# Performance work log

Measured on AMD Instinct MI355X. Metric: run time of the kernel, lower is better.

Reference implementation:

```python
import jax, jax.numpy as jnp
import numpy as np

G, T, V, K = 24, 2048, 2048, 512  # group size, seq len, vocab, hidden


def setup_inputs() -> dict:
    key = jax.random.key(0)
    k1, k2, k3, k4 = jax.random.split(key, 4)
    # one-hot input sequence (T, V), batch squeezed away as in the torch code
    tokens = jax.random.randint(k1, (T,), 0, V)
    sequence = jax.nn.one_hot(tokens, V, dtype=jnp.float32)
    # group represented as V-permutations (one per group element); cyclic shifts
    # give a valid faithful permutation representation for the reference
    perms = (jnp.arange(V)[None, :] + jnp.arange(G)[:, None] * (V // G)) % V
    W_e = jax.random.normal(k2, (V, K), jnp.float32) * 0.02          # WordConv embedding table
    Wx = jax.random.normal(k3, (K, K), jnp.float32) / np.sqrt(K)     # input-to-hidden (shared across g)
    Wh = jax.random.normal(k4, (K, K), jnp.float32) / np.sqrt(K)     # hidden-to-hidden (shared across g)
    b = jnp.zeros((K,), jnp.float32)
    return {"sequence": sequence, "perms": perms, "W_e": W_e, "Wx": Wx, "Wh": Wh, "b": b}


def _forward_pass(xproj, Wh):
    # xproj: (T, G, K) pre-computed input projections; GRNN recurrence per group copy
    h0 = jnp.zeros(xproj.shape[1:], xproj.dtype)  # (G, K)

    def step(h, x):
        h = jnp.tanh(x + h @ Wh)
        return h, h

    hT, hs = jax.lax.scan(step, h0, xproj)
    return hs, hT  # (T, G, K), (G, K)


def reference(sequence, perms, W_e, Wx, Wh, b):
    # WordConv group embedding: emb[t, g] = W_e[perm_g(token_t)] via one-hot matmul
    emb = jnp.einsum('tv,gvk->tgk', sequence, W_e[perms])  # (T, G, K)
    xproj = jnp.einsum('tgk,kh->tgh', emb, Wx) + b         # hoist input GEMM out of the scan
    hid_f, ht_f = _forward_pass(xproj, Wh)
    # bidirectional: reverse = cat(seq[:-1].flip(0), seq[-1][None]) exactly as in torch
    rev = jnp.concatenate([xproj[:-1][::-1], xproj[-1:]], axis=0)
    hid_b, ht_b = _forward_pass(rev, Wh)
    hid_b = jnp.concatenate([hid_b[:-1][::-1], hid_b[-1:]], axis=0)
    hidden_all = jnp.concatenate([hid_f, hid_b], axis=-1)  # (T, G, 2K)
    ht = jnp.concatenate([ht_f, ht_b], axis=-1)            # (G, 2K)
    return hidden_all, ht
```

## Files before the change

### kernel.cpp

```cpp
#include <hip/hip_runtime.h>

#define T_LEN 2048
#define G_N   24
#define V_N   2048
#define K_N   512
#define NCL   48
#define NBLK  96

#define TOK_OFF    4096
#define ROWS_OFF   16384
#define HBUF_OFF   262144
#define P_OFF      786432

#define LOAD_RLX64(p)     __hip_atomic_load((p), __ATOMIC_RELAXED, __HIP_MEMORY_SCOPE_AGENT)
#define STORE_RLX64(p, v) __hip_atomic_store((p), (v), __ATOMIC_RELAXED, __HIP_MEMORY_SCOPE_AGENT)

#define BAR_LDS() do {                                         \
    asm volatile("s_waitcnt lgkmcnt(0)" ::: "memory");         \
    __builtin_amdgcn_s_barrier();                              \
    asm volatile("" ::: "memory");                             \
} while (0)

__global__ void tok_kernel(const float* __restrict__ seq, int* __restrict__ tokens) {
    int wid  = (blockIdx.x * blockDim.x + threadIdx.x) >> 6;
    int lane = threadIdx.x & 63;
    if (wid >= T_LEN) return;
    const float* row = seq + (size_t)wid * V_N;
    for (int i = lane; i < V_N; i += 64) {
        if (row[i] > 0.5f) tokens[wid] = i;
    }
}

__global__ void rows_kernel(const int* __restrict__ tokens, const int* __restrict__ perms,
                            int* __restrict__ rows) {
    int idx = blockIdx.x * blockDim.x + threadIdx.x;
    if (idx >= G_N * T_LEN) return;
    int g = idx / T_LEN, t = idx - g * T_LEN;
    rows[idx] = perms[g * V_N + tokens[t]];
}

__global__ __launch_bounds__(256) void pgemm_kernel(const float* __restrict__ We,
                                                    const float* __restrict__ Wx,
                                                    const float* __restrict__ b,
                                                    float* __restrict__ P) {
    __shared__ float As[16][72];
    __shared__ float Bs[16][68];
    int tid = threadIdx.x;
    int bx = blockIdx.x & 7;
    int by = blockIdx.x >> 3;
    int tx = tid & 15, ty = tid >> 4;
    int v0 = by * 64, j0 = bx * 64;
    float acc[4][4] = {};
    for (int k0 = 0; k0 < K_N; k0 += 16) {
        int ar = tid >> 2;
        int ac = (tid & 3) << 2;
        float4 av = *(const float4*)(We + (size_t)(v0 + ar) * K_N + k0 + ac);
        As[ac + 0][ar] = av.x; As[ac + 1][ar] = av.y;
        As[ac + 2][ar] = av.z; As[ac + 3][ar] = av.w;
        int br = tid >> 4;
        int bc = (tid & 15) << 2;
        float4 bv = *(const float4*)(Wx + (size_t)(k0 + br) * K_N + j0 + bc);
        *(float4*)&Bs[br][bc] = bv;
        __syncthreads();
#pragma unroll
        for (int kk = 0; kk < 16; kk++) {
            float a0 = As[kk][ty * 4 + 0], a1 = As[kk][ty * 4 + 1];
            float a2 = As[kk][ty * 4 + 2], a3 = As[kk][ty * 4 + 3];
            float4 bb = *(const float4*)&Bs[kk][tx * 4];
            acc[0][0] += a0 * bb.x; acc[0][1] += a0 * bb.y; acc[0][2] += a0 * bb.z; acc[0][3] += a0 * bb.w;
            acc[1][0] += a1 * bb.x; acc[1][1] += a1 * bb.y; acc[1][2] += a1 * bb.z; acc[1][3] += a1 * bb.w;
            acc[2][0] += a2 * bb.x; acc[2][1] += a2 * bb.y; acc[2][2] += a2 * bb.z; acc[2][3] += a2 * bb.w;
            acc[3][0] += a3 * bb.x; acc[3][1] += a3 * bb.y; acc[3][2] += a3 * bb.z; acc[3][3] += a3 * bb.w;
        }
        __syncthreads();
    }
    float4 bb = *(const float4*)(b + j0 + tx * 4);
#pragma unroll
    for (int i = 0; i < 4; i++) {
        float4 r;
        r.x = acc[i][0] + bb.x; r.y = acc[i][1] + bb.y;
        r.z = acc[i][2] + bb.z; r.w = acc[i][3] + bb.w;
        *(float4*)(P + (size_t)(v0 + ty * 4 + i) * K_N + j0 + tx * 4) = r;
    }
}

__global__ __attribute__((amdgpu_flat_work_group_size(512, 512), amdgpu_waves_per_eu(2, 2)))
void rnn_pair(const float* __restrict__ P, const float* __restrict__ Wh,
              const int* __restrict__ rows, unsigned long long* __restrict__ h_buf,
              float* __restrict__ out) {

    __shared__ __align__(16) float  lds_h[K_N];
    __shared__ __align__(16) float4 Wlds[16 * 512];
    __shared__ __align__(16) float  pr[8 * 264];

    const int tid = threadIdx.x;
    const int q   = tid >> 6;
    const int cluster = blockIdx.x >> 1;
    const int ws  = blockIdx.x & 1;
    const int g   = cluster >> 1;
    const int dir = cluster & 1;

    const int ownbase = ws << 8;
    const int pbase   = ownbase ^ 256;
    const int wcol    = (ws << 6) + (tid & 63);

    const float4* __restrict__ Wh4 = (const float4*)Wh;

    float4 Wreg[48];
#pragma unroll
    for (int ph = 0; ph < 2; ph++) {
        const int kb = (ph == 0 ? ownbase : pbase) + (q << 5);
#pragma unroll
        for (int i = 0; i < 32; i++) {
            float4 w = Wh4[(size_t)(kb + i) * 128 + wcol];
            if (i < 8) Wlds[(ph * 8 + i) * 512 + tid] = w;
            else       Wreg[ph * 24 + (i - 8)] = w;
        }
    }
    lds_h[tid] = 0.f;

    const int* __restrict__ myrows = rows + g * T_LEN;
    int t0 = (dir == 0) ? 0 : (T_LEN - 2);
    float xv = (tid < 256) ? P[(size_t)myrows[t0] * K_N + ownbase + tid] : 0.f;
    int t1 = (dir == 0) ? 1 : (T_LEN - 3);
    int rnxt = myrows[t1];

    unsigned long long* hbme = h_buf + ((size_t)cluster * 2 + ws) * 512;
    unsigned long long* hbpt = h_buf + ((size_t)cluster * 2 + (ws ^ 1)) * 512;

    const size_t outbase = (size_t)g * 1024 + (size_t)dir * 512 + ownbase + tid;
    float h_prev = 0.f;
    size_t prev_addr = 0;

    __syncthreads();

    for (int s = 0; s < T_LEN; s++) {
        unsigned long long pvbits = 0;
        if (s > 0 && tid < 256)
            pvbits = LOAD_RLX64(&hbpt[((s - 1) & 1) * 256 + tid]);

        if (s > 0 && tid < 256) __builtin_nontemporal_store(h_prev, &out[prev_addr]);
        float xv_next = 0.f;
        if (tid < 256 && s + 1 < T_LEN) xv_next = P[(size_t)rnxt * K_N + ownbase + tid];
        if (s + 2 < T_LEN) {
            int sn = s + 2;
            int tn = (dir == 0) ? sn : ((sn == T_LEN - 1) ? (T_LEN - 1) : (T_LEN - 2 - sn));
            rnxt = myrows[tn];
        }

        const float4* __restrict__ h4 = (const float4*)lds_h;
        float4 acc = {0.f, 0.f, 0.f, 0.f};

        {
            const int hb = (ownbase >> 2) + (q << 3);
#pragma unroll
            for (int r8 = 0; r8 < 8; r8++) {
                float4 hv = h4[hb + r8];
#pragma unroll
                for (int e = 0; e < 4; e++) {
                    float hs = (e == 0) ? hv.x : (e == 1) ? hv.y : (e == 2) ? hv.z : hv.w;
                    const int i = 4 * r8 + e;
                    float4 w = (i < 8) ? Wlds[i * 512 + tid] : Wreg[i - 8];
                    acc.x += hs * w.x; acc.y += hs * w.y; acc.z += hs * w.z; acc.w += hs * w.w;
                }
            }
        }
        if (s > 0 && tid < 256) {
            while ((unsigned)(pvbits >> 32) != (unsigned)s)
                pvbits = LOAD_RLX64(&hbpt[((s - 1) & 1) * 256 + tid]);
            lds_h[pbase + tid] = __uint_as_float((unsigned)pvbits);
        }
        BAR_LDS();

        {
            const int hb = (pbase >> 2) + (q << 3);
#pragma unroll
            for (int r8 = 0; r8 < 8; r8++) {
                float4 hv = h4[hb + r8];
#pragma unroll
                for (int e = 0; e < 4; e++) {
                    float hs = (e == 0) ? hv.x : (e == 1) ? hv.y : (e == 2) ? hv.z : hv.w;
                    const int i = 4 * r8 + e;
                    float4 w = (i < 8) ? Wlds[(8 + i) * 512 + tid] : Wreg[24 + i - 8];
                    acc.x += hs * w.x; acc.y += hs * w.y; acc.z += hs * w.z; acc.w += hs * w.w;
                }
            }
        }
        *(float4*)&pr[q * 264 + 4 * (tid & 63)] = acc;
        BAR_LDS();

        if (tid < 256) {
            float p0 = pr[0 * 264 + tid], p1 = pr[1 * 264 + tid];
            float p2 = pr[2 * 264 + tid], p3 = pr[3 * 264 + tid];
            float p4 = pr[4 * 264 + tid], p5 = pr[5 * 264 + tid];
            float p6 = pr[6 * 264 + tid], p7 = pr[7 * 264 + tid];
            float sum = ((p0 + p1) + (p2 + p3)) + ((p4 + p5) + (p6 + p7));
            float z = xv + sum;
            z = fminf(15.f, fmaxf(-15.f, z));
            float e2 = __expf(2.f * z);
            float h1 = 1.f - 2.f / (e2 + 1.f);
            xv = xv_next;

            int tphys = (dir == 0) ? s : ((s == T_LEN - 1) ? (T_LEN - 1) : (T_LEN - 2 - s));
            prev_addr = (size_t)tphys * (G_N * 1024) + outbase;
            h_prev = h1;
            if (s < T_LEN - 1) {
                unsigned long long pk =
                    ((unsigned long long)(unsigned)(s + 1) << 32) | __float_as_uint(h1);
                STORE_RLX64(&hbme[(s & 1) * 256 + tid], pk);
                lds_h[ownbase + tid] = h1;
            }
        }
        if (s == T_LEN - 1) break;
        BAR_LDS();
    }
    if (tid < 256) {
        __builtin_nontemporal_store(h_prev, &out[prev_addr]);
        __builtin_nontemporal_store(h_prev, &out[(size_t)T_LEN * (G_N * 1024) + outbase]);
    }
}

extern "C" void kernel_launch(void* const* d_in, const int* in_sizes, int n_in,
                              void* d_out, int out_size, void* d_ws, size_t ws_size,
                              hipStream_t stream) {
    const float* seq   = (const float*)d_in[0];
    const int*   perms = (const int*)d_in[1];
    const float* We    = (const float*)d_in[2];
    const float* Wx    = (const float*)d_in[3];
    const float* Wh    = (const float*)d_in[4];
    const float* b     = (const float*)d_in[5];
    float* out = (float*)d_out;
    char* ws = (char*)d_ws;

    int*   tokens = (int*)(ws + TOK_OFF);
    int*   rows   = (int*)(ws + ROWS_OFF);
    unsigned long long* hbuf = (unsigned long long*)(ws + HBUF_OFF);
    float* P      = (float*)(ws + P_OFF);

    (void)hipMemsetAsync(hbuf, 0, NCL * 2 * 2 * 256 * sizeof(unsigned long long), stream);
    tok_kernel<<<512, 256, 0, stream>>>(seq, tokens);
    rows_kernel<<<(G_N * T_LEN + 255) / 256, 256, 0, stream>>>(tokens, perms, rows);
    pgemm_kernel<<<256, 256, 0, stream>>>(We, Wx, b, P);
    rnn_pair<<<NBLK, 512, 0, stream>>>(P, Wh, rows, hbuf, out);
}
```

Measured before the change: 5.772 ms.

## Fuse forward and backward recurrences into one block pair sharing Wh

Each two-block cluster now runs both the forward and the backward chain of a group at once, so the launch drops from 96 blocks to 48. Every Wh weight loaded from registers or LDS feeds two independent FMA chains, one per direction. All 512 threads now take part in the reduction, tanh and exchange stages, where only 256 did before. The cost is twice the FMA work per thread each step and double the LDS buffers for hidden state and partial sums. This only helps if the per-step time is set by the exchange latency between blocks rather than by arithmetic.

```diff
diff --git a/kernel.cpp b/kernel.cpp
--- a/kernel.cpp
+++ b/kernel.cpp
@@ -5,7 +5,7 @@
 #define V_N   2048
 #define K_N   512
 #define NCL   48
-#define NBLK  96
+#define NBLK  48
 
 #define TOK_OFF    4096
 #define ROWS_OFF   16384
@@ -85,24 +85,25 @@
 }
 
 __global__ __attribute__((amdgpu_flat_work_group_size(512, 512), amdgpu_waves_per_eu(2, 2)))
-void rnn_pair(const float* __restrict__ P, const float* __restrict__ Wh,
+void rnn_bidi(const float* __restrict__ P, const float* __restrict__ Wh,
               const int* __restrict__ rows, unsigned long long* __restrict__ h_buf,
               float* __restrict__ out) {
 
-    __shared__ __align__(16) float  lds_h[K_N];
+    __shared__ __align__(16) float  lds_h[2 * K_N];
     __shared__ __align__(16) float4 Wlds[16 * 512];
-    __shared__ __align__(16) float  pr[8 * 264];
+    __shared__ __align__(16) float  pr[16 * 264];
 
     const int tid = threadIdx.x;
     const int q   = tid >> 6;
-    const int cluster = blockIdx.x >> 1;
+    const int c   = tid & 63;
+    const int g   = blockIdx.x >> 1;
     const int ws  = blockIdx.x & 1;
-    const int g   = cluster >> 1;
-    const int dir = cluster & 1;
+    const int chain = tid >> 8;
+    const int lc    = tid & 255;
 
     const int ownbase = ws << 8;
     const int pbase   = ownbase ^ 256;
-    const int wcol    = (ws << 6) + (tid & 63);
+    const int wcol    = (ws << 6) + c;
 
     const float4* __restrict__ Wh4 = (const float4*)Wh;
 
@@ -118,17 +119,18 @@
         }
     }
     lds_h[tid] = 0.f;
+    lds_h[512 + tid] = 0.f;
 
     const int* __restrict__ myrows = rows + g * T_LEN;
-    int t0 = (dir == 0) ? 0 : (T_LEN - 2);
-    float xv = (tid < 256) ? P[(size_t)myrows[t0] * K_N + ownbase + tid] : 0.f;
-    int t1 = (dir == 0) ? 1 : (T_LEN - 3);
+    int t0 = (chain == 0) ? 0 : (T_LEN - 2);
+    float xv = P[(size_t)myrows[t0] * K_N + ownbase + lc];
+    int t1 = (chain == 0) ? 1 : (T_LEN - 3);
     int rnxt = myrows[t1];
 
-    unsigned long long* hbme = h_buf + ((size_t)cluster * 2 + ws) * 512;
-    unsigned long long* hbpt = h_buf + ((size_t)cluster * 2 + (ws ^ 1)) * 512;
-
-    const size_t outbase = (size_t)g * 1024 + (size_t)dir * 512 + ownbase + tid;
+    unsigned long long* hbme = h_buf + ((size_t)(g * 2 + chain) * 2 + ws) * 512;
+    unsigned long long* hbpt = h_buf + ((size_t)(g * 2 + chain) * 2 + (ws ^ 1)) * 512;
+
+    const size_t outbase = (size_t)g * 1024 + (size_t)chain * 512 + ownbase + lc;
     float h_prev = 0.f;
     size_t prev_addr = 0;
 
@@ -136,39 +138,43 @@
 
     for (int s = 0; s < T_LEN; s++) {
         unsigned long long pvbits = 0;
-        if (s > 0 && tid < 256)
-            pvbits = LOAD_RLX64(&hbpt[((s - 1) & 1) * 256 + tid]);
-
-        if (s > 0 && tid < 256) __builtin_nontemporal_store(h_prev, &out[prev_addr]);
+        if (s > 0)
+            pvbits = LOAD_RLX64(&hbpt[((s - 1) & 1) * 256 + lc]);
+
+        if (s > 0) __builtin_nontemporal_store(h_prev, &out[prev_addr]);
         float xv_next = 0.f;
-        if (tid < 256 && s + 1 < T_LEN) xv_next = P[(size_t)rnxt * K_N + ownbase + tid];
+        if (s + 1 < T_LEN) xv_next = P[(size_t)rnxt * K_N + ownbase + lc];
         if (s + 2 < T_LEN) {
             int sn = s + 2;
-            int tn = (dir == 0) ? sn : ((sn == T_LEN - 1) ? (T_LEN - 1) : (T_LEN - 2 - sn));
+            int tn = (chain == 0) ? sn : ((sn == T_LEN - 1) ? (T_LEN - 1) : (T_LEN - 2 - sn));
             rnxt = myrows[tn];
         }
 
-        const float4* __restrict__ h4 = (const float4*)lds_h;
-        float4 acc = {0.f, 0.f, 0.f, 0.f};
+        const float4* __restrict__ h4f = (const float4*)lds_h;
+        const float4* __restrict__ h4b = (const float4*)(lds_h + 512);
+        float4 af = {0.f, 0.f, 0.f, 0.f}, ab = {0.f, 0.f, 0.f, 0.f};
 
         {
             const int hb = (ownbase >> 2) + (q << 3);
 #pragma unroll
             for (int r8 = 0; r8 < 8; r8++) {
-                float4 hv = h4[hb + r8];
+                float4 hf = h4f[hb + r8];
+                float4 hbv = h4b[hb + r8];
 #pragma unroll
                 for (int e = 0; e < 4; e++) {
-                    float hs = (e == 0) ? hv.x : (e == 1) ? hv.y : (e == 2) ? hv.z : hv.w;
+                    float sf = (e == 0) ? hf.x : (e == 1) ? hf.y : (e == 2) ? hf.z : hf.w;
+                    float sb = (e == 0) ? hbv.x : (e == 1) ? hbv.y : (e == 2) ? hbv.z : hbv.w;
                     const int i = 4 * r8 + e;
                     float4 w = (i < 8) ? Wlds[i * 512 + tid] : Wreg[i - 8];
-                    acc.x += hs * w.x; acc.y += hs * w.y; acc.z += hs * w.z; acc.w += hs * w.w;
+                    af.x += sf * w.x; af.y += sf * w.y; af.z += sf * w.z; af.w += sf * w.w;
+                    ab.x += sb * w.x; ab.y += sb * w.y; ab.z += sb * w.z; ab.w += sb * w.w;
                 }
             }
         }
-        if (s > 0 && tid < 256) {
+        if (s > 0) {
             while ((unsigned)(pvbits >> 32) != (unsigned)s)
-                pvbits = LOAD_RLX64(&hbpt[((s - 1) & 1) * 256 + tid]);
-            lds_h[pbase + tid] = __uint_as_float((unsigned)pvbits);
+                pvbits = LOAD_RLX64(&hbpt[((s - 1) & 1) * 256 + lc]);
+            lds_h[chain * 512 + pbase + lc] = __uint_as_float((unsigned)pvbits);
         }
         BAR_LDS();
 
@@ -176,24 +182,29 @@
             const int hb = (pbase >> 2) + (q << 3);
 #pragma unroll
             for (int r8 = 0; r8 < 8; r8++) {
-                float4 hv = h4[hb + r8];
+                float4 hf = h4f[hb + r8];
+                float4 hbv = h4b[hb + r8];
 #pragma unroll
                 for (int e = 0; e < 4; e++) {
-                    float hs = (e == 0) ? hv.x : (e == 1) ? hv.y : (e == 2) ? hv.z : hv.w;
+                    float sf = (e == 0) ? hf.x : (e == 1) ? hf.y : (e == 2) ? hf.z : hf.w;
+                    float sb = (e == 0) ? hbv.x : (e == 1) ? hbv.y : (e == 2) ? hbv.z : hbv.w;
                     const int i = 4 * r8 + e;
                     float4 w = (i < 8) ? Wlds[(8 + i) * 512 + tid] : Wreg[24 + i - 8];
-                    acc.x += hs * w.x; acc.y += hs * w.y; acc.z += hs * w.z; acc.w += hs * w.w;
+                    af.x += sf * w.x; af.y += sf * w.y; af.z += sf * w.z; af.w += sf * w.w;
+                    ab.x += sb * w.x; ab.y += sb * w.y; ab.z += sb * w.z; ab.w += sb * w.w;
                 }
             }
         }
-        *(float4*)&pr[q * 264 + 4 * (tid & 63)] = acc;
+        *(float4*)&pr[q * 264 + 4 * c] = af;
+        *(float4*)&pr[(8 + q) * 264 + 4 * c] = ab;
         BAR_LDS();
 
-        if (tid < 256) {
-            float p0 = pr[0 * 264 + tid], p1 = pr[1 * 264 + tid];
-            float p2 = pr[2 * 264 + tid], p3 = pr[3 * 264 + tid];
-            float p4 = pr[4 * 264 + tid], p5 = pr[5 * 264 + tid];
-            float p6 = pr[6 * 264 + tid], p7 = pr[7 * 264 + tid];
+        {
+            const float* prc = pr + chain * 8 * 264;
+            float p0 = prc[0 * 264 + lc], p1 = prc[1 * 264 + lc];
+            float p2 = prc[2 * 264 + lc], p3 = prc[3 * 264 + lc];
+            float p4 = prc[4 * 264 + lc], p5 = prc[5 * 264 + lc];
+            float p6 = prc[6 * 264 + lc], p7 = prc[7 * 264 + lc];
             float sum = ((p0 + p1) + (p2 + p3)) + ((p4 + p5) + (p6 + p7));
             float z = xv + sum;
             z = fminf(15.f, fmaxf(-15.f, z));
@@ -201,23 +212,21 @@
             float h1 = 1.f - 2.f / (e2 + 1.f);
             xv = xv_next;
 
-            int tphys = (dir == 0) ? s : ((s == T_LEN - 1) ? (T_LEN - 1) : (T_LEN - 2 - s));
+            int tphys = (chain == 0) ? s : ((s == T_LEN - 1) ? (T_LEN - 1) : (T_LEN - 2 - s));
             prev_addr = (size_t)tphys * (G_N * 1024) + outbase;
             h_prev = h1;
             if (s < T_LEN - 1) {
                 unsigned long long pk =
                     ((unsigned long long)(unsigned)(s + 1) << 32) | __float_as_uint(h1);
-                STORE_RLX64(&hbme[(s & 1) * 256 + tid], pk);
-                lds_h[ownbase + tid] = h1;
+                STORE_RLX64(&hbme[(s & 1) * 256 + lc], pk);
+                lds_h[chain * 512 + ownbase + lc] = h1;
             }
         }
         if (s == T_LEN - 1) break;
         BAR_LDS();
     }
-    if (tid < 256) {
-        __builtin_nontemporal_store(h_prev, &out[prev_addr]);
-        __builtin_nontemporal_store(h_prev, &out[(size_t)T_LEN * (G_N * 1024) + outbase]);
-    }
+    __builtin_nontemporal_store(h_prev, &out[prev_addr]);
+    __builtin_nontemporal_store(h_prev, &out[(size_t)T_LEN * (G_N * 1024) + outbase]);
 }
 
 extern "C" void kernel_launch(void* const* d_in, const int* in_sizes, int n_in,
@@ -241,5 +250,5 @@
     tok_kernel<<<512, 256, 0, stream>>>(seq, tokens);
     rows_kernel<<<(G_N * T_LEN + 255) / 256, 256, 0, stream>>>(tokens, perms, rows);
     pgemm_kernel<<<256, 256, 0, stream>>>(We, Wx, b, P);
-    rnn_pair<<<NBLK, 512, 0, stream>>>(P, Wh, rows, hbuf, out);
-}
+    rnn_bidi<<<NBLK, 512, 0, stream>>>(P, Wh, rows, hbuf, out);
+}
```

Result: slower. 13.12 ms (+127.3%).

## Split recurrence matvec 2x2 across four blocks sharing Wh tile for both directions

Applied to the files above, without the earlier changes.

Each group now uses four blocks, each owning a 256x256 quadrant of Wh held entirely in registers. Every block computes partial products for both the forward and backward directions, then exchanges the partial sums through global memory flags. Previously a block pair split the hidden units of one direction and exchanged full h halves, keeping part of Wh in LDS. The goal is to drop the LDS weight reads and lower per-block work per step. The cost is a three-way cross-block wait every step and redundant tanh evaluation.

```diff
diff --git a/kernel.cpp b/kernel.cpp
--- a/kernel.cpp
+++ b/kernel.cpp
@@ -4,13 +4,12 @@
 #define G_N   24
 #define V_N   2048
 #define K_N   512
-#define NCL   48
 #define NBLK  96
 
 #define TOK_OFF    4096
 #define ROWS_OFF   16384
 #define HBUF_OFF   262144
-#define P_OFF      786432
+#define P_OFF      1048576
 
 #define LOAD_RLX64(p)     __hip_atomic_load((p), __ATOMIC_RELAXED, __HIP_MEMORY_SCOPE_AGENT)
 #define STORE_RLX64(p, v) __hip_atomic_store((p), (v), __ATOMIC_RELAXED, __HIP_MEMORY_SCOPE_AGENT)
@@ -85,136 +84,139 @@
 }
 
 __global__ __attribute__((amdgpu_flat_work_group_size(512, 512), amdgpu_waves_per_eu(2, 2)))
-void rnn_pair(const float* __restrict__ P, const float* __restrict__ Wh,
+void rnn_quad(const float* __restrict__ P, const float* __restrict__ Wh,
               const int* __restrict__ rows, unsigned long long* __restrict__ h_buf,
               float* __restrict__ out) {
 
-    __shared__ __align__(16) float  lds_h[K_N];
-    __shared__ __align__(16) float4 Wlds[16 * 512];
-    __shared__ __align__(16) float  pr[8 * 264];
+    __shared__ __align__(16) float lds_h[2][512];
+    __shared__ __align__(16) float pr[2][8][264];
 
     const int tid = threadIdx.x;
-    const int q   = tid >> 6;
-    const int cluster = blockIdx.x >> 1;
-    const int ws  = blockIdx.x & 1;
-    const int g   = cluster >> 1;
-    const int dir = cluster & 1;
-
-    const int ownbase = ws << 8;
-    const int pbase   = ownbase ^ 256;
-    const int wcol    = (ws << 6) + (tid & 63);
+    const int fc  = tid & 63;
+    const int kq  = tid >> 6;
+    const int g   = blockIdx.x >> 2;
+    const int RB  = (blockIdx.x >> 1) & 1;
+    const int CB  = blockIdx.x & 1;
+    const int d_r = tid >> 8;
+    const int lc  = tid & 255;
 
     const float4* __restrict__ Wh4 = (const float4*)Wh;
-
-    float4 Wreg[48];
-#pragma unroll
-    for (int ph = 0; ph < 2; ph++) {
-        const int kb = (ph == 0 ? ownbase : pbase) + (q << 5);
-#pragma unroll
-        for (int i = 0; i < 32; i++) {
-            float4 w = Wh4[(size_t)(kb + i) * 128 + wcol];
-            if (i < 8) Wlds[(ph * 8 + i) * 512 + tid] = w;
-            else       Wreg[ph * 24 + (i - 8)] = w;
-        }
-    }
-    lds_h[tid] = 0.f;
+    const int rowbase = (RB << 8) + (kq << 5);
+    float4 Wreg[32];
+#pragma unroll
+    for (int i = 0; i < 32; i++)
+        Wreg[i] = Wh4[(size_t)(rowbase + i) * 128 + (CB << 6) + fc];
+
+    lds_h[0][tid] = 0.f;
+    lds_h[1][tid] = 0.f;
 
     const int* __restrict__ myrows = rows + g * T_LEN;
-    int t0 = (dir == 0) ? 0 : (T_LEN - 2);
-    float xv = (tid < 256) ? P[(size_t)myrows[t0] * K_N + ownbase + tid] : 0.f;
-    int t1 = (dir == 0) ? 1 : (T_LEN - 3);
+    int t0 = (d_r == 0) ? 0 : (T_LEN - 2);
+    float xv0 = P[(size_t)myrows[t0] * K_N + lc];
+    float xv1 = P[(size_t)myrows[t0] * K_N + lc + 256];
+    int t1 = (d_r == 0) ? 1 : (T_LEN - 3);
     int rnxt = myrows[t1];
 
-    unsigned long long* hbme = h_buf + ((size_t)cluster * 2 + ws) * 512;
-    unsigned long long* hbpt = h_buf + ((size_t)cluster * 2 + (ws ^ 1)) * 512;
-
-    const size_t outbase = (size_t)g * 1024 + (size_t)dir * 512 + ownbase + tid;
+#define BUF(dd, rb, cb) (h_buf + ((((size_t)g * 2 + (dd)) * 2 + (rb)) * 2 + (cb)) * 2 * 256)
+    unsigned long long* bown = BUF(d_r, RB, CB);
+    unsigned long long* brem0 = BUF(d_r, RB ^ 1, CB);
+    unsigned long long* brem1 = BUF(d_r, 0, CB ^ 1);
+    unsigned long long* brem2 = BUF(d_r, 1, CB ^ 1);
+
+    const int writer = (d_r == RB);
+    const size_t outbase = (size_t)g * 1024 + (size_t)RB * 512 + (CB << 8) + lc;
     float h_prev = 0.f;
     size_t prev_addr = 0;
 
     __syncthreads();
 
     for (int s = 0; s < T_LEN; s++) {
-        unsigned long long pvbits = 0;
-        if (s > 0 && tid < 256)
-            pvbits = LOAD_RLX64(&hbpt[((s - 1) & 1) * 256 + tid]);
-
-        if (s > 0 && tid < 256) __builtin_nontemporal_store(h_prev, &out[prev_addr]);
-        float xv_next = 0.f;
-        if (tid < 256 && s + 1 < T_LEN) xv_next = P[(size_t)rnxt * K_N + ownbase + tid];
+        if (s > 0 && writer) __builtin_nontemporal_store(h_prev, &out[prev_addr]);
+        float xn0 = 0.f, xn1 = 0.f;
+        if (s + 1 < T_LEN) {
+            xn0 = P[(size_t)rnxt * K_N + lc];
+            xn1 = P[(size_t)rnxt * K_N + lc + 256];
+        }
         if (s + 2 < T_LEN) {
             int sn = s + 2;
-            int tn = (dir == 0) ? sn : ((sn == T_LEN - 1) ? (T_LEN - 1) : (T_LEN - 2 - sn));
+            int tn = (d_r == 0) ? sn : ((sn == T_LEN - 1) ? (T_LEN - 1) : (T_LEN - 2 - sn));
             rnxt = myrows[tn];
         }
 
-        const float4* __restrict__ h4 = (const float4*)lds_h;
-        float4 acc = {0.f, 0.f, 0.f, 0.f};
-
+        const float4* __restrict__ lh4 = (const float4*)lds_h;
+        const int hb = (RB << 6) + (kq << 3);
+        float4 af = {0.f, 0.f, 0.f, 0.f}, ab = {0.f, 0.f, 0.f, 0.f};
+#pragma unroll
+        for (int r8 = 0; r8 < 8; r8++) {
+            float4 hf = lh4[hb + r8];
+            float4 hv = lh4[128 + hb + r8];
+#pragma unroll
+            for (int e = 0; e < 4; e++) {
+                float sf = (e == 0) ? hf.x : (e == 1) ? hf.y : (e == 2) ? hf.z : hf.w;
+                float sb = (e == 0) ? hv.x : (e == 1) ? hv.y : (e == 2) ? hv.z : hv.w;
+                float4 w = Wreg[4 * r8 + e];
+                af.x += sf * w.x; af.y += sf * w.y; af.z += sf * w.z; af.w += sf * w.w;
+                ab.x += sb * w.x; ab.y += sb * w.y; ab.z += sb * w.z; ab.w += sb * w.w;
+            }
+        }
+        *(float4*)&pr[0][kq][4 * fc] = af;
+        *(float4*)&pr[1][kq][4 * fc] = ab;
+        BAR_LDS();
+
+        float p0 = pr[d_r][0][lc], p1 = pr[d_r][1][lc];
+        float p2 = pr[d_r][2][lc], p3 = pr[d_r][3][lc];
+        float p4 = pr[d_r][4][lc], p5 = pr[d_r][5][lc];
+        float p6 = pr[d_r][6][lc], p7 = pr[d_r][7][lc];
+        float own_p = ((p0 + p1) + (p2 + p3)) + ((p4 + p5) + (p6 + p7));
         {
-            const int hb = (ownbase >> 2) + (q << 3);
-#pragma unroll
-            for (int r8 = 0; r8 < 8; r8++) {
-                float4 hv = h4[hb + r8];
-#pragma unroll
-                for (int e = 0; e < 4; e++) {
-                    float hs = (e == 0) ? hv.x : (e == 1) ? hv.y : (e == 2) ? hv.z : hv.w;
-                    const int i = 4 * r8 + e;
-                    float4 w = (i < 8) ? Wlds[i * 512 + tid] : Wreg[i - 8];
-                    acc.x += hs * w.x; acc.y += hs * w.y; acc.z += hs * w.z; acc.w += hs * w.w;
-                }
-            }
-        }
-        if (s > 0 && tid < 256) {
-            while ((unsigned)(pvbits >> 32) != (unsigned)s)
-                pvbits = LOAD_RLX64(&hbpt[((s - 1) & 1) * 256 + tid]);
-            lds_h[pbase + tid] = __uint_as_float((unsigned)pvbits);
-        }
-        BAR_LDS();
-
-        {
-            const int hb = (pbase >> 2) + (q << 3);
-#pragma unroll
-            for (int r8 = 0; r8 < 8; r8++) {
-                float4 hv = h4[hb + r8];
-#pragma unroll
-                for (int e = 0; e < 4; e++) {
-                    float hs = (e == 0) ? hv.x : (e == 1) ? hv.y : (e == 2) ? hv.z : hv.w;
-                    const int i = 4 * r8 + e;
-                    float4 w = (i < 8) ? Wlds[(8 + i) * 512 + tid] : Wreg[24 + i - 8];
-                    acc.x += hs * w.x; acc.y += hs * w.y; acc.z += hs * w.z; acc.w += hs * w.w;
-                }
-            }
-        }
-        *(float4*)&pr[q * 264 + 4 * (tid & 63)] = acc;
-        BAR_LDS();
-
-        if (tid < 256) {
-            float p0 = pr[0 * 264 + tid], p1 = pr[1 * 264 + tid];
-            float p2 = pr[2 * 264 + tid], p3 = pr[3 * 264 + tid];
-            float p4 = pr[4 * 264 + tid], p5 = pr[5 * 264 + tid];
-            float p6 = pr[6 * 264 + tid], p7 = pr[7 * 264 + tid];
-            float sum = ((p0 + p1) + (p2 + p3)) + ((p4 + p5) + (p6 + p7));
-            float z = xv + sum;
-            z = fminf(15.f, fmaxf(-15.f, z));
-            float e2 = __expf(2.f * z);
-            float h1 = 1.f - 2.f / (e2 + 1.f);
-            xv = xv_next;
-
-            int tphys = (dir == 0) ? s : ((s == T_LEN - 1) ? (T_LEN - 1) : (T_LEN - 2 - s));
+            unsigned long long pk =
+                ((unsigned long long)(unsigned)(s + 1) << 32) | __float_as_uint(own_p);
+            STORE_RLX64(&bown[(s & 1) * 256 + lc], pk);
+        }
+
+        unsigned long long e0 = LOAD_RLX64(&brem0[(s & 1) * 256 + lc]);
+        unsigned long long e1 = LOAD_RLX64(&brem1[(s & 1) * 256 + lc]);
+        unsigned long long e2 = LOAD_RLX64(&brem2[(s & 1) * 256 + lc]);
+        while ((unsigned)(e0 >> 32) != (unsigned)(s + 1))
+            e0 = LOAD_RLX64(&brem0[(s & 1) * 256 + lc]);
+        while ((unsigned)(e1 >> 32) != (unsigned)(s + 1))
+            e1 = LOAD_RLX64(&brem1[(s & 1) * 256 + lc]);
+        while ((unsigned)(e2 >> 32) != (unsigned)(s + 1))
+            e2 = LOAD_RLX64(&brem2[(s & 1) * 256 + lc]);
+        float r0 = __uint_as_float((unsigned)e0);
+        float r1 = __uint_as_float((unsigned)e1);
+        float r2 = __uint_as_float((unsigned)e2);
+
+        float c0a, c0b, c1a, c1b;
+        if (CB == 0) {
+            c0a = (RB == 0) ? own_p : r0;  c0b = (RB == 0) ? r0 : own_p;
+            c1a = r1;                      c1b = r2;
+        } else {
+            c1a = (RB == 0) ? own_p : r0;  c1b = (RB == 0) ? r0 : own_p;
+            c0a = r1;                      c0b = r2;
+        }
+        float z0 = xv0 + (c0a + c0b);
+        z0 = fminf(15.f, fmaxf(-15.f, z0));
+        float ee0 = __expf(2.f * z0);
+        float h0 = 1.f - 2.f / (ee0 + 1.f);
+        float z1 = xv1 + (c1a + c1b);
+        z1 = fminf(15.f, fmaxf(-15.f, z1));
+        float ee1 = __expf(2.f * z1);
+        float h1 = 1.f - 2.f / (ee1 + 1.f);
+        xv0 = xn0; xv1 = xn1;
+
+        lds_h[d_r][lc] = h0;
+        lds_h[d_r][lc + 256] = h1;
+
+        if (writer) {
+            int tphys = (d_r == 0) ? s : ((s == T_LEN - 1) ? (T_LEN - 1) : (T_LEN - 2 - s));
             prev_addr = (size_t)tphys * (G_N * 1024) + outbase;
-            h_prev = h1;
-            if (s < T_LEN - 1) {
-                unsigned long long pk =
-                    ((unsigned long long)(unsigned)(s + 1) << 32) | __float_as_uint(h1);
-                STORE_RLX64(&hbme[(s & 1) * 256 + tid], pk);
-                lds_h[ownbase + tid] = h1;
-            }
+            h_prev = (CB == 0) ? h0 : h1;
         }
         if (s == T_LEN - 1) break;
         BAR_LDS();
     }
-    if (tid < 256) {
+    if (writer) {
         __builtin_nontemporal_store(h_prev, &out[prev_addr]);
         __builtin_nontemporal_store(h_prev, &out[(size_t)T_LEN * (G_N * 1024) + outbase]);
     }
@@ -237,9 +239,9 @@
     unsigned long long* hbuf = (unsigned long long*)(ws + HBUF_OFF);
     float* P      = (float*)(ws + P_OFF);
 
-    (void)hipMemsetAsync(hbuf, 0, NCL * 2 * 2 * 256 * sizeof(unsigned long long), stream);
+    (void)hipMemsetAsync(hbuf, 0, (size_t)G_N * 2 * 2 * 2 * 2 * 256 * sizeof(unsigned long long), stream);
     tok_kernel<<<512, 256, 0, stream>>>(seq, tokens);
     rows_kernel<<<(G_N * T_LEN + 255) / 256, 256, 0, stream>>>(tokens, perms, rows);
     pgemm_kernel<<<256, 256, 0, stream>>>(We, Wx, b, P);
-    rnn_pair<<<NBLK, 512, 0, stream>>>(P, Wh, rows, hbuf, out);
-}
+    rnn_quad<<<NBLK, 512, 0, stream>>>(P, Wh, rows, hbuf, out);
+}
```

Measured after the change: 5.192 ms. 10.0% less time.
